# Performance work log

Measured on AMD Instinct MI355X. Metric: run time of the kernel, lower is better.

The kernel has to match this reference:

```python
import jax, jax.numpy as jnp
import numpy as np

B, T, D = 4, 4096, 256
N_SCALES, N_EXPERTS = 3, 4
KERNELS = [5, 9, 17]           # kernel bank, one group of N_EXPERTS experts per size
E = N_SCALES * N_EXPERTS       # 12 total experts
EPS = 1e-5


def _dw_causal_conv(x, w):
    """Depthwise causal conv over time. x:[B,T,D], w:[k,D] -> [B,T,D]."""
    k = w.shape[0]
    xp = jnp.pad(x, ((0, 0), (k - 1, 0), (0, 0)))
    return jax.lax.conv_general_dilated(
        xp, w[:, None, :], window_strides=(1,), padding='VALID',
        dimension_numbers=('NWC', 'WIO', 'NWC'), feature_group_count=x.shape[-1])


def setup_inputs() -> dict:
    key = jax.random.key(0)
    ks = jax.random.split(key, 12)
    s = 0.02
    return {
        'x':       jax.random.normal(ks[0], (B, T, D), jnp.float32),
        'conv_k5':  jax.random.normal(ks[1], (N_EXPERTS, 5, D), jnp.float32) * s,
        'conv_k9':  jax.random.normal(ks[2], (N_EXPERTS, 9, D), jnp.float32) * s,
        'conv_k17': jax.random.normal(ks[3], (N_EXPERTS, 17, D), jnp.float32) * s,
        'proj_W':   jax.random.normal(ks[4], (E, D, D), jnp.float32) * s,
        'proj_b':   jnp.zeros((E, D), jnp.float32),
        'router_W': jax.random.normal(ks[5], (D, E), jnp.float32) * s,
        'router_b': jnp.zeros((E,), jnp.float32),
        'out_W':    jax.random.normal(ks[6], (D, D), jnp.float32) * s,
        'out_b':    jnp.zeros((D,), jnp.float32),
        'gamma':    jnp.ones((D,), jnp.float32),
        'beta':     jnp.zeros((D,), jnp.float32),
    }


def reference(x, conv_k5, conv_k9, conv_k17, proj_W, proj_b,
              router_W, router_b, out_W, out_b, gamma, beta):
    # per-scale expert SSM (causal depthwise conv), vmapped over the 4 experts per size
    ssm_out = jnp.concatenate([
        jax.vmap(lambda w: _dw_causal_conv(x, w))(conv_k5),
        jax.vmap(lambda w: _dw_causal_conv(x, w))(conv_k9),
        jax.vmap(lambda w: _dw_causal_conv(x, w))(conv_k17),
    ], axis=0)                                             # [E,B,T,D]
    # per-expert linear projection -> [B,T,E,D]
    stack = jnp.einsum('ebtd,edf->btef', ssm_out, proj_W) + proj_b
    # router: convex combination over E experts per token
    weights = jax.nn.softmax(x @ router_W + router_b, axis=-1)   # [B,T,E]
    mixed = jnp.einsum('btef,bte->btf', stack, weights)          # [B,T,D]
    # LayerNorm
    mu = jnp.mean(mixed, axis=-1, keepdims=True)
    var = jnp.var(mixed, axis=-1, keepdims=True)
    normed = (mixed - mu) * jax.lax.rsqrt(var + EPS) * gamma + beta
    return normed @ out_W + out_b
```

## Files before the change

### kernel.cpp

```cpp
#include <hip/hip_runtime.h>
#include <hip/hip_bf16.h>

typedef short short8 __attribute__((ext_vector_type(8)));
typedef short short4_t __attribute__((ext_vector_type(4)));
typedef float floatx4 __attribute__((ext_vector_type(4)));

#define DEVI __device__ __forceinline__


DEVI float bf2f(__hip_bfloat16 v) { return __bfloat162float(v); }
DEVI __hip_bfloat16 f2bf(float v) { return __float2bfloat16(v); }
DEVI unsigned short bfbits(float v) { __hip_bfloat16 b = f2bf(v); return *(unsigned short*)&b; }

__global__ __launch_bounds__(256) void prep_kernel(
    const float* __restrict__ rW,
    const float* __restrict__ projW,
    const float* __restrict__ outW,
    const float* __restrict__ projb,
    __hip_bfloat16* __restrict__ projWT,
    __hip_bfloat16* __restrict__ outWT,
    __hip_bfloat16* __restrict__ projbT,
    __hip_bfloat16* __restrict__ rWT)
{
    __shared__ __align__(16) __hip_bfloat16 Tt[64 * 72];
    const int bid = blockIdx.x;
    const int tid = threadIdx.x;

    if (bid == 208) {
#pragma unroll
        for (int k = 0; k < 32; k++)
            projbT[tid * 32 + k] = (k < 12) ? f2bf(projb[k * 256 + tid]) : f2bf(0.f);
#pragma unroll
        for (int e = 0; e < 16; e++)
            rWT[e * 256 + tid] = (e < 12) ? f2bf(rW[tid * 12 + e]) : f2bf(0.f);
        return;
    }
    const float* src;
    __hip_bfloat16* dst;
    if (bid < 192) {
        int e = bid >> 4, ti = (bid & 15) >> 2, tj = bid & 3;
        src = projW + (e << 16) + (ti * 64) * 256 + tj * 64;
        dst = projWT + (e << 16) + (tj * 64) * 256 + ti * 64;
    } else {
        int b3 = bid - 192, ti = b3 >> 2, tj = b3 & 3;
        src = outW + (ti * 64) * 256 + tj * 64;
        dst = outWT + (tj * 64) * 256 + ti * 64;
    }
#pragma unroll
    for (int i = 0; i < 4; i++) {
        int r = i * 16 + (tid >> 4);
        int c4 = (tid & 15) * 4;
        float4 f = *(const float4*)(src + r * 256 + c4);
        Tt[(c4 + 0) * 72 + r] = f2bf(f.x);
        Tt[(c4 + 1) * 72 + r] = f2bf(f.y);
        Tt[(c4 + 2) * 72 + r] = f2bf(f.z);
        Tt[(c4 + 3) * 72 + r] = f2bf(f.w);
    }
    __syncthreads();
#pragma unroll
    for (int i = 0; i < 2; i++) {
        int c = i * 32 + (tid >> 3);
        int r8 = (tid & 7) * 8;
        *(short8*)(dst + c * 256 + r8) = *(const short8*)(Tt + c * 72 + r8);
    }
}

constexpr int SMEM_BYTES = 118016;

template<int K>
DEVI void conv_lds2(const float2 (&cf)[17], const unsigned* __restrict__ xsu,
                    int tloc, int du, const float4 (&wt4)[4],
                    unsigned* __restrict__ dp)
{
    unsigned w[16];
#pragma unroll
    for (int i = 0; i < K - 1; i++)
        w[i] = xsu[(16 + tloc - (K - 1) + i) * 132 + du];
#pragma unroll
    for (int t = 0; t < 16; t++) {
        unsigned nv = xsu[(16 + tloc + t) * 132 + du];
        float y0 = cf[K - 1].x * __uint_as_float(nv << 16);
        float y1 = cf[K - 1].y * __uint_as_float(nv & 0xffff0000u);
#pragma unroll
        for (int i = 0; i < K - 1; i++) {
            y0 = fmaf(cf[i].x, __uint_as_float(w[i] << 16), y0);
            y1 = fmaf(cf[i].y, __uint_as_float(w[i] & 0xffff0000u), y1);
        }
        float wt = wt4[t >> 2][t & 3];
        unsigned pv = ((unsigned)bfbits(y1 * wt) << 16) | (unsigned)bfbits(y0 * wt);
        dp[t * 132] = pv;
#pragma unroll
        for (int i = 0; i + 1 < K - 1; i++) w[i] = w[i + 1];
        if (K > 1) w[K - 2] = nv;
    }
}

template<int NKS>
DEVI void gemm_inl(const __hip_bfloat16* __restrict__ A, int astride,
                   const __hip_bfloat16* __restrict__ Bg, int bstride,
                   floatx4 (&acc)[4][2], int l16, int quad, int nsl)
{
    const __hip_bfloat16* ap = A + l16 * astride + quad * 8;
    const __hip_bfloat16* bp = Bg + (nsl + l16) * bstride + quad * 8;
    short8 a[4], b[2];
#pragma unroll
    for (int mf = 0; mf < 4; mf++) a[mf] = *(const short8*)(ap + mf * 16 * astride);
#pragma unroll
    for (int nt = 0; nt < 2; nt++) b[nt] = *(const short8*)(bp + nt * 16 * bstride);
#pragma unroll
    for (int ks = 0; ks < NKS; ks++) {
        short8 na[4], nb[2];
        if (ks < NKS - 1) {
#pragma unroll
            for (int mf = 0; mf < 4; mf++)
                na[mf] = *(const short8*)(ap + mf * 16 * astride + (ks + 1) * 32);
#pragma unroll
            for (int nt = 0; nt < 2; nt++)
                nb[nt] = *(const short8*)(bp + nt * 16 * bstride + (ks + 1) * 32);
        }
#pragma unroll
        for (int nt = 0; nt < 2; nt++)
#pragma unroll
            for (int mf = 0; mf < 4; mf++)
                acc[mf][nt] = __builtin_amdgcn_mfma_f32_16x16x32_bf16(
                    a[mf], b[nt], acc[mf][nt], 0, 0, 0);
        if (ks < NKS - 1) {
#pragma unroll
            for (int mf = 0; mf < 4; mf++) a[mf] = na[mf];
#pragma unroll
            for (int nt = 0; nt < 2; nt++) b[nt] = nb[nt];
        }
    }
}

__global__ __launch_bounds__(512, 1) void fused_kernel(
    const float* __restrict__ x,
    const float* __restrict__ ck5, const float* __restrict__ ck9,
    const float* __restrict__ ck17,
    const float* __restrict__ rb,
    const float* __restrict__ gmm, const float* __restrict__ bta,
    const float* __restrict__ outb,
    const __hip_bfloat16* __restrict__ projWT,
    const __hip_bfloat16* __restrict__ outWT,
    const __hip_bfloat16* __restrict__ projbT,
    const __hip_bfloat16* __restrict__ rWT,
    float* __restrict__ out)
{
    extern __shared__ char smem[];
    __hip_bfloat16* xs   = (__hip_bfloat16*)smem;
    __hip_bfloat16* bufA = (__hip_bfloat16*)(smem + 42240);
    __hip_bfloat16* bufB = (__hip_bfloat16*)(smem + 76032);
    float* wts_s = (float*)(smem + 109824);
    float* psum  = (float*)(smem + 112896);
    float* psq   = (float*)(smem + 115200);
    float* muA   = (float*)(smem + 117504);
    float* rsA   = (float*)(smem + 117760);
    const unsigned* xsu = (const unsigned*)xs;

    const int tid  = threadIdx.x;
    const int wave = tid >> 6;
    const int lane = tid & 63;
    const int quad = lane >> 4;
    const int l16  = lane & 15;
    const int nsl  = wave * 32;
    const bool gemmFirst = (wave >= 4);
    const int m0   = blockIdx.x * 64;
    const int bb   = m0 >> 12;
    const int t0   = m0 & 4095;

    {
        const float* xb = x + (size_t)bb * 4096 * 256;
        for (int idx = tid; idx < 80 * 64; idx += 512) {
            int row = idx >> 6, c4 = (idx & 63) << 2;
            int gt = t0 - 16 + row;
            short4_t v = {0, 0, 0, 0};
            if (gt >= 0) {
                float4 f = *(const float4*)(xb + (size_t)gt * 256 + c4);
                v[0] = (short)bfbits(f.x); v[1] = (short)bfbits(f.y);
                v[2] = (short)bfbits(f.z); v[3] = (short)bfbits(f.w);
            }
            *(short4_t*)(xs + row * 264 + c4) = v;
        }
    }
    __syncthreads();

    if (wave < 4) {
        floatx4 ra = {0.f, 0.f, 0.f, 0.f};
        const __hip_bfloat16* ap = xs + (16 + wave * 16 + l16) * 264 + quad * 8;
        const __hip_bfloat16* bp = rWT + l16 * 256 + quad * 8;
#pragma unroll
        for (int kk = 0; kk < 256; kk += 32)
            ra = __builtin_amdgcn_mfma_f32_16x16x32_bf16(
                *(const short8*)(ap + kk), *(const short8*)(bp + kk), ra, 0, 0, 0);
        float rbv = (l16 < 12) ? rb[l16] : 0.f;
#pragma unroll
        for (int r = 0; r < 4; r++) {
            float v = (l16 < 12) ? (ra[r] + rbv) : -1e30f;
            float mx = v;
            mx = fmaxf(mx, __shfl_xor(mx, 1));
            mx = fmaxf(mx, __shfl_xor(mx, 2));
            mx = fmaxf(mx, __shfl_xor(mx, 4));
            mx = fmaxf(mx, __shfl_xor(mx, 8));
            float ex = (l16 < 12) ? __expf(v - mx) : 0.f;
            float sm = ex;
            sm += __shfl_xor(sm, 1);
            sm += __shfl_xor(sm, 2);
            sm += __shfl_xor(sm, 4);
            sm += __shfl_xor(sm, 8);
            if (l16 < 12) wts_s[l16 * 64 + (wave * 16 + quad * 4 + r)] = ex / sm;
        }
    }
    __syncthreads();

    const int d0   = 2 * (tid & 127);
    const int du   = d0 >> 1;
    const int tloc = (tid >> 7) * 16;

    auto loadCoef = [&](float2 (&cf)[17], int e) {
        if (e < 4) {
            const float* cw = ck5 + e * 5 * 256;
#pragma unroll
            for (int j = 0; j < 17; j++)
                cf[j] = (j < 5) ? *(const float2*)(cw + j * 256 + d0) : make_float2(0.f, 0.f);
        } else if (e < 8) {
            const float* cw = ck9 + (e - 4) * 9 * 256;
#pragma unroll
            for (int j = 0; j < 17; j++)
                cf[j] = (j < 9) ? *(const float2*)(cw + j * 256 + d0) : make_float2(0.f, 0.f);
        } else {
            const float* cw = ck17 + (e - 8) * 17 * 256;
#pragma unroll
            for (int j = 0; j < 17; j++)
                cf[j] = *(const float2*)(cw + j * 256 + d0);
        }
    };
    auto produce = [&](int e, __hip_bfloat16* dst) {
        float2 cf[17];
        loadCoef(cf, e);
        float4 wt4[4];
#pragma unroll
        for (int g = 0; g < 4; g++)
            wt4[g] = *(const float4*)(wts_s + e * 64 + tloc + 4 * g);
        unsigned* dp = (unsigned*)dst + tloc * 132 + du;
        if (e < 4)      conv_lds2<5>(cf, xsu, tloc, du, wt4, dp);
        else if (e < 8) conv_lds2<9>(cf, xsu, tloc, du, wt4, dp);
        else            conv_lds2<17>(cf, xsu, tloc, du, wt4, dp);
    };
    auto produceBias = [&](__hip_bfloat16* dst) {
        int t = tid >> 3, k4 = (tid & 7) * 4;
        short4_t v;
#pragma unroll
        for (int j = 0; j < 4; j++) {
            int k = k4 + j;
            v[j] = (k < 12) ? (short)bfbits(wts_s[k * 64 + t]) : (short)0;
        }
        *(short4_t*)(dst + t * 264 + k4) = v;
    };

    floatx4 acc[4][2];
#pragma unroll
    for (int i = 0; i < 4; i++)
#pragma unroll
        for (int j = 0; j < 2; j++) acc[i][j] = {0.f, 0.f, 0.f, 0.f};

    __hip_bfloat16* bufC = bufA;
    __hip_bfloat16* bufN = bufB;

    produce(0, bufC);
    __syncthreads();

#pragma unroll 1
    for (int r = 0; r < 11; r++) {
        const __hip_bfloat16* Bg = projWT + ((size_t)r << 16);
        if (gemmFirst) {
            gemm_inl<8>(bufC, 264, Bg, 256, acc, l16, quad, nsl);
            produce(r + 1, bufN);
        } else {
            produce(r + 1, bufN);
            gemm_inl<8>(bufC, 264, Bg, 256, acc, l16, quad, nsl);
        }
        { __hip_bfloat16* t_ = bufC; bufC = bufN; bufN = t_; }
        __syncthreads();
    }
    {
        const __hip_bfloat16* Bg = projWT + ((size_t)11 << 16);
        if (gemmFirst) {
            gemm_inl<8>(bufC, 264, Bg, 256, acc, l16, quad, nsl);
            produceBias(bufN);
        } else {
            produceBias(bufN);
            gemm_inl<8>(bufC, 264, Bg, 256, acc, l16, quad, nsl);
        }
        { __hip_bfloat16* t_ = bufC; bufC = bufN; bufN = t_; }
        __syncthreads();
    }
    gemm_inl<1>(bufC, 264, projbT, 32, acc, l16, quad, nsl);

    {
        float s[16], s2[16];
#pragma unroll
        for (int mf = 0; mf < 4; mf++)
#pragma unroll
            for (int r = 0; r < 4; r++) {
                int i = mf * 4 + r;
                float v = 0.f, q = 0.f;
#pragma unroll
                for (int nt = 0; nt < 2; nt++) {
                    float a = acc[mf][nt][r];
                    v += a; q += a * a;
                }
                s[i] = v; s2[i] = q;
            }
#pragma unroll
        for (int m = 1; m <= 8; m <<= 1)
#pragma unroll
            for (int i = 0; i < 16; i++) {
                s[i]  += __shfl_xor(s[i], m);
                s2[i] += __shfl_xor(s2[i], m);
            }
#pragma unroll
        for (int i = 0; i < 16; i++)
            if (l16 == i) {
                int row = (i >> 2) * 16 + quad * 4 + (i & 3);
                psum[row * 9 + wave] = s[i];
                psq[row * 9 + wave]  = s2[i];
            }
    }
    __syncthreads();
    if (tid < 64) {
        float ss = 0.f, qq = 0.f;
#pragma unroll
        for (int p = 0; p < 8; p++) { ss += psum[tid * 9 + p]; qq += psq[tid * 9 + p]; }
        float mu = ss * 0.00390625f;
        float var = fmaxf(qq * 0.00390625f - mu * mu, 0.f);
        muA[tid] = mu;
        rsA[tid] = rsqrtf(var + 1e-5f);
    }
    __syncthreads();

    __hip_bfloat16* normed = bufN;
#pragma unroll
    for (int nt = 0; nt < 2; nt++) {
        int col = nsl + nt * 16 + l16;
        float g = gmm[col], bt = bta[col];
#pragma unroll
        for (int mf = 0; mf < 4; mf++)
#pragma unroll
            for (int r = 0; r < 4; r++) {
                int row = mf * 16 + quad * 4 + r;
                normed[row * 264 + col] =
                    f2bf((acc[mf][nt][r] - muA[row]) * rsA[row] * g + bt);
            }
    }
    __syncthreads();

    floatx4 acc2[4][2];
#pragma unroll
    for (int i = 0; i < 4; i++)
#pragma unroll
        for (int j = 0; j < 2; j++) acc2[i][j] = {0.f, 0.f, 0.f, 0.f};
    gemm_inl<8>(normed, 264, outWT, 256, acc2, l16, quad, nsl);

    float* op = out + (size_t)m0 * 256;
#pragma unroll
    for (int nt = 0; nt < 2; nt++) {
        int col = nsl + nt * 16 + l16;
        float ob = outb[col];
#pragma unroll
        for (int mf = 0; mf < 4; mf++)
#pragma unroll
            for (int r = 0; r < 4; r++) {
                int row = mf * 16 + quad * 4 + r;
                op[row * 256 + col] = acc2[mf][nt][r] + ob;
            }
    }
}

extern "C" void kernel_launch(void* const* d_in, const int* in_sizes, int n_in,
                              void* d_out, int out_size, void* d_ws, size_t ws_size,
                              hipStream_t stream)
{
    (void)in_sizes; (void)n_in; (void)out_size; (void)ws_size;
    const float* x     = (const float*)d_in[0];
    const float* ck5   = (const float*)d_in[1];
    const float* ck9   = (const float*)d_in[2];
    const float* ck17  = (const float*)d_in[3];
    const float* projW = (const float*)d_in[4];
    const float* projb = (const float*)d_in[5];
    const float* rW    = (const float*)d_in[6];
    const float* rb    = (const float*)d_in[7];
    const float* outW  = (const float*)d_in[8];
    const float* outb  = (const float*)d_in[9];
    const float* gmm   = (const float*)d_in[10];
    const float* bta   = (const float*)d_in[11];

    __hip_bfloat16* projWT = (__hip_bfloat16*)d_ws;
    __hip_bfloat16* outWT  = (__hip_bfloat16*)((char*)d_ws + 1572864);
    __hip_bfloat16* projbT = (__hip_bfloat16*)((char*)d_ws + 1703936);
    __hip_bfloat16* rWT    = (__hip_bfloat16*)((char*)d_ws + 1720320);

    static bool attr_set = false;
    if (!attr_set) {
        hipFuncSetAttribute((const void*)fused_kernel,
                            hipFuncAttributeMaxDynamicSharedMemorySize, SMEM_BYTES);
        attr_set = true;
    }

    prep_kernel<<<dim3(209), dim3(256), 0, stream>>>(
        rW, projW, outW, projb, projWT, outWT, projbT, rWT);
    fused_kernel<<<dim3(256), dim3(512), SMEM_BYTES, stream>>>(
        x, ck5, ck9, ck17, rb, gmm, bta, outb,
        projWT, outWT, projbT, rWT, (float*)d_out);
}
```

Baseline: 174.6 us.

## Double block size to 1024 threads, splitting GEMM M rows and conv time rows

Launches the fused kernel with 16 waves instead of 8. Each wave now owns a 32x32 output tile (the M dimension is split into two halves) instead of 64x32, and each conv thread processes 8 timesteps instead of 16. The aim is more latency hiding and parallelism per CU, since only 256 blocks run, one per CU. In exchange, each wave does less work per B-fragment load, so B-operand traffic from global/L2 is duplicated across the two M halves, and the register budget per thread shrinks.

After: 221.2 us. 1.27x slower.

```diff
diff --git a/kernel.cpp b/kernel.cpp
--- a/kernel.cpp
+++ b/kernel.cpp
@@ -67,9 +67,9 @@
 
 constexpr int SMEM_BYTES = 118016;
 
-template<int K>
+template<int K, int NT>
 DEVI void conv_lds2(const float2 (&cf)[17], const unsigned* __restrict__ xsu,
-                    int tloc, int du, const float4 (&wt4)[4],
+                    int tloc, int du, const float4 (&wt4)[NT / 4],
                     unsigned* __restrict__ dp)
 {
     unsigned w[16];
@@ -77,7 +77,7 @@
     for (int i = 0; i < K - 1; i++)
         w[i] = xsu[(16 + tloc - (K - 1) + i) * 132 + du];
 #pragma unroll
-    for (int t = 0; t < 16; t++) {
+    for (int t = 0; t < NT; t++) {
         unsigned nv = xsu[(16 + tloc + t) * 132 + du];
         float y0 = cf[K - 1].x * __uint_as_float(nv << 16);
         float y1 = cf[K - 1].y * __uint_as_float(nv & 0xffff0000u);
@@ -98,21 +98,21 @@
 template<int NKS>
 DEVI void gemm_inl(const __hip_bfloat16* __restrict__ A, int astride,
                    const __hip_bfloat16* __restrict__ Bg, int bstride,
-                   floatx4 (&acc)[4][2], int l16, int quad, int nsl)
+                   floatx4 (&acc)[2][2], int l16, int quad, int mh, int ns)
 {
-    const __hip_bfloat16* ap = A + l16 * astride + quad * 8;
-    const __hip_bfloat16* bp = Bg + (nsl + l16) * bstride + quad * 8;
-    short8 a[4], b[2];
-#pragma unroll
-    for (int mf = 0; mf < 4; mf++) a[mf] = *(const short8*)(ap + mf * 16 * astride);
+    const __hip_bfloat16* ap = A + (mh * 32 + l16) * astride + quad * 8;
+    const __hip_bfloat16* bp = Bg + (ns * 32 + l16) * bstride + quad * 8;
+    short8 a[2], b[2];
+#pragma unroll
+    for (int mf = 0; mf < 2; mf++) a[mf] = *(const short8*)(ap + mf * 16 * astride);
 #pragma unroll
     for (int nt = 0; nt < 2; nt++) b[nt] = *(const short8*)(bp + nt * 16 * bstride);
 #pragma unroll
     for (int ks = 0; ks < NKS; ks++) {
-        short8 na[4], nb[2];
+        short8 na[2], nb[2];
         if (ks < NKS - 1) {
 #pragma unroll
-            for (int mf = 0; mf < 4; mf++)
+            for (int mf = 0; mf < 2; mf++)
                 na[mf] = *(const short8*)(ap + mf * 16 * astride + (ks + 1) * 32);
 #pragma unroll
             for (int nt = 0; nt < 2; nt++)
@@ -121,19 +121,19 @@
 #pragma unroll
         for (int nt = 0; nt < 2; nt++)
 #pragma unroll
-            for (int mf = 0; mf < 4; mf++)
+            for (int mf = 0; mf < 2; mf++)
                 acc[mf][nt] = __builtin_amdgcn_mfma_f32_16x16x32_bf16(
                     a[mf], b[nt], acc[mf][nt], 0, 0, 0);
         if (ks < NKS - 1) {
 #pragma unroll
-            for (int mf = 0; mf < 4; mf++) a[mf] = na[mf];
+            for (int mf = 0; mf < 2; mf++) a[mf] = na[mf];
 #pragma unroll
             for (int nt = 0; nt < 2; nt++) b[nt] = nb[nt];
         }
     }
 }
 
-__global__ __launch_bounds__(512, 1) void fused_kernel(
+__global__ __launch_bounds__(1024, 1) void fused_kernel(
     const float* __restrict__ x,
     const float* __restrict__ ck5, const float* __restrict__ ck9,
     const float* __restrict__ ck17,
@@ -162,15 +162,16 @@
     const int lane = tid & 63;
     const int quad = lane >> 4;
     const int l16  = lane & 15;
-    const int nsl  = wave * 32;
-    const bool gemmFirst = (wave >= 4);
+    const int mh   = wave >> 3;
+    const int ns   = wave & 7;
+    const bool gemmFirst = ((wave >> 2) & 1);
     const int m0   = blockIdx.x * 64;
     const int bb   = m0 >> 12;
     const int t0   = m0 & 4095;
 
     {
         const float* xb = x + (size_t)bb * 4096 * 256;
-        for (int idx = tid; idx < 80 * 64; idx += 512) {
+        for (int idx = tid; idx < 80 * 64; idx += 1024) {
             int row = idx >> 6, c4 = (idx & 63) << 2;
             int gt = t0 - 16 + row;
             short4_t v = {0, 0, 0, 0};
@@ -214,7 +215,7 @@
 
     const int d0   = 2 * (tid & 127);
     const int du   = d0 >> 1;
-    const int tloc = (tid >> 7) * 16;
+    const int tloc = (tid >> 7) * 8;
 
     auto loadCoef = [&](float2 (&cf)[17], int e) {
         if (e < 4) {
@@ -237,29 +238,31 @@
     auto produce = [&](int e, __hip_bfloat16* dst) {
         float2 cf[17];
         loadCoef(cf, e);
-        float4 wt4[4];
-#pragma unroll
-        for (int g = 0; g < 4; g++)
+        float4 wt4[2];
+#pragma unroll
+        for (int g = 0; g < 2; g++)
             wt4[g] = *(const float4*)(wts_s + e * 64 + tloc + 4 * g);
         unsigned* dp = (unsigned*)dst + tloc * 132 + du;
-        if (e < 4)      conv_lds2<5>(cf, xsu, tloc, du, wt4, dp);
-        else if (e < 8) conv_lds2<9>(cf, xsu, tloc, du, wt4, dp);
-        else            conv_lds2<17>(cf, xsu, tloc, du, wt4, dp);
+        if (e < 4)      conv_lds2<5, 8>(cf, xsu, tloc, du, wt4, dp);
+        else if (e < 8) conv_lds2<9, 8>(cf, xsu, tloc, du, wt4, dp);
+        else            conv_lds2<17, 8>(cf, xsu, tloc, du, wt4, dp);
     };
     auto produceBias = [&](__hip_bfloat16* dst) {
-        int t = tid >> 3, k4 = (tid & 7) * 4;
-        short4_t v;
-#pragma unroll
-        for (int j = 0; j < 4; j++) {
-            int k = k4 + j;
-            v[j] = (k < 12) ? (short)bfbits(wts_s[k * 64 + t]) : (short)0;
-        }
-        *(short4_t*)(dst + t * 264 + k4) = v;
+        if (tid < 512) {
+            int t = tid >> 3, k4 = (tid & 7) * 4;
+            short4_t v;
+#pragma unroll
+            for (int j = 0; j < 4; j++) {
+                int k = k4 + j;
+                v[j] = (k < 12) ? (short)bfbits(wts_s[k * 64 + t]) : (short)0;
+            }
+            *(short4_t*)(dst + t * 264 + k4) = v;
+        }
     };
 
-    floatx4 acc[4][2];
-#pragma unroll
-    for (int i = 0; i < 4; i++)
+    floatx4 acc[2][2];
+#pragma unroll
+    for (int i = 0; i < 2; i++)
 #pragma unroll
         for (int j = 0; j < 2; j++) acc[i][j] = {0.f, 0.f, 0.f, 0.f};
 
@@ -273,11 +276,11 @@
     for (int r = 0; r < 11; r++) {
         const __hip_bfloat16* Bg = projWT + ((size_t)r << 16);
         if (gemmFirst) {
-            gemm_inl<8>(bufC, 264, Bg, 256, acc, l16, quad, nsl);
+            gemm_inl<8>(bufC, 264, Bg, 256, acc, l16, quad, mh, ns);
             produce(r + 1, bufN);
         } else {
             produce(r + 1, bufN);
-            gemm_inl<8>(bufC, 264, Bg, 256, acc, l16, quad, nsl);
+            gemm_inl<8>(bufC, 264, Bg, 256, acc, l16, quad, mh, ns);
         }
         { __hip_bfloat16* t_ = bufC; bufC = bufN; bufN = t_; }
         __syncthreads();
@@ -285,21 +288,21 @@
     {
         const __hip_bfloat16* Bg = projWT + ((size_t)11 << 16);
         if (gemmFirst) {
-            gemm_inl<8>(bufC, 264, Bg, 256, acc, l16, quad, nsl);
+            gemm_inl<8>(bufC, 264, Bg, 256, acc, l16, quad, mh, ns);
             produceBias(bufN);
         } else {
             produceBias(bufN);
-            gemm_inl<8>(bufC, 264, Bg, 256, acc, l16, quad, nsl);
+            gemm_inl<8>(bufC, 264, Bg, 256, acc, l16, quad, mh, ns);
         }
         { __hip_bfloat16* t_ = bufC; bufC = bufN; bufN = t_; }
         __syncthreads();
     }
-    gemm_inl<1>(bufC, 264, projbT, 32, acc, l16, quad, nsl);
+    gemm_inl<1>(bufC, 264, projbT, 32, acc, l16, quad, mh, ns);
 
     {
-        float s[16], s2[16];
-#pragma unroll
-        for (int mf = 0; mf < 4; mf++)
+        float s[8], s2[8];
+#pragma unroll
+        for (int mf = 0; mf < 2; mf++)
 #pragma unroll
             for (int r = 0; r < 4; r++) {
                 int i = mf * 4 + r;
@@ -314,16 +317,16 @@
 #pragma unroll
         for (int m = 1; m <= 8; m <<= 1)
 #pragma unroll
-            for (int i = 0; i < 16; i++) {
+            for (int i = 0; i < 8; i++) {
                 s[i]  += __shfl_xor(s[i], m);
                 s2[i] += __shfl_xor(s2[i], m);
             }
 #pragma unroll
-        for (int i = 0; i < 16; i++)
+        for (int i = 0; i < 8; i++)
             if (l16 == i) {
-                int row = (i >> 2) * 16 + quad * 4 + (i & 3);
-                psum[row * 9 + wave] = s[i];
-                psq[row * 9 + wave]  = s2[i];
+                int row = mh * 32 + (i >> 2) * 16 + quad * 4 + (i & 3);
+                psum[row * 9 + ns] = s[i];
+                psq[row * 9 + ns]  = s2[i];
             }
     }
     __syncthreads();
@@ -341,36 +344,36 @@
     __hip_bfloat16* normed = bufN;
 #pragma unroll
     for (int nt = 0; nt < 2; nt++) {
-        int col = nsl + nt * 16 + l16;
+        int col = ns * 32 + nt * 16 + l16;
         float g = gmm[col], bt = bta[col];
 #pragma unroll
-        for (int mf = 0; mf < 4; mf++)
+        for (int mf = 0; mf < 2; mf++)
 #pragma unroll
             for (int r = 0; r < 4; r++) {
-                int row = mf * 16 + quad * 4 + r;
+                int row = mh * 32 + mf * 16 + quad * 4 + r;
                 normed[row * 264 + col] =
                     f2bf((acc[mf][nt][r] - muA[row]) * rsA[row] * g + bt);
             }
     }
     __syncthreads();
 
-    floatx4 acc2[4][2];
-#pragma unroll
-    for (int i = 0; i < 4; i++)
+    floatx4 acc2[2][2];
+#pragma unroll
+    for (int i = 0; i < 2; i++)
 #pragma unroll
         for (int j = 0; j < 2; j++) acc2[i][j] = {0.f, 0.f, 0.f, 0.f};
-    gemm_inl<8>(normed, 264, outWT, 256, acc2, l16, quad, nsl);
+    gemm_inl<8>(normed, 264, outWT, 256, acc2, l16, quad, mh, ns);
 
     float* op = out + (size_t)m0 * 256;
 #pragma unroll
     for (int nt = 0; nt < 2; nt++) {
-        int col = nsl + nt * 16 + l16;
+        int col = ns * 32 + nt * 16 + l16;
         float ob = outb[col];
 #pragma unroll
-        for (int mf = 0; mf < 4; mf++)
+        for (int mf = 0; mf < 2; mf++)
 #pragma unroll
             for (int r = 0; r < 4; r++) {
-                int row = mf * 16 + quad * 4 + r;
+                int row = mh * 32 + mf * 16 + quad * 4 + r;
                 op[row * 256 + col] = acc2[mf][nt][r] + ob;
             }
     }
@@ -408,7 +411,7 @@
 
     prep_kernel<<<dim3(209), dim3(256), 0, stream>>>(
         rW, projW, outW, projb, projWT, outWT, projbT, rWT);
-    fused_kernel<<<dim3(256), dim3(512), SMEM_BYTES, stream>>>(
+    fused_kernel<<<dim3(256), dim3(1024), SMEM_BYTES, stream>>>(
         x, ck5, ck9, ck17, rb, gmm, bta, outb,
         projWT, outWT, projbT, rWT, (float*)d_out);
 }
```

## Halve row tile to 32 with 256-thread blocks and drop double buffering

Applied to the files above, without the earlier changes.

Shrinks each block from 64 rows/512 threads to 32 rows/256 threads, doubling the grid to 512 blocks. The per-wave tile changes from 4x2 to 2x4 MFMA fragments. The double-buffered produce/GEMM overlap across wave groups is replaced by a single LDS buffer with two barriers per expert, so LDS drops to about 45KB and two blocks can share a CU. This trades intra-block overlap of conv and GEMM for more resident blocks and better CU coverage. It also doubles how often the projection weights are re-read per token.

Result: slower. 208.0 us (+19.1%).

```diff
diff --git a/kernel.cpp b/kernel.cpp
--- a/kernel.cpp
+++ b/kernel.cpp
@@ -65,7 +65,6 @@
     }
 }
 
-constexpr int SMEM_BYTES = 118016;
 
 template<int K>
 DEVI void conv_lds2(const float2 (&cf)[17], const unsigned* __restrict__ xsu,
@@ -98,42 +97,42 @@
 template<int NKS>
 DEVI void gemm_inl(const __hip_bfloat16* __restrict__ A, int astride,
                    const __hip_bfloat16* __restrict__ Bg, int bstride,
-                   floatx4 (&acc)[4][2], int l16, int quad, int nsl)
+                   floatx4 (&acc)[2][4], int l16, int quad, int nsl)
 {
     const __hip_bfloat16* ap = A + l16 * astride + quad * 8;
     const __hip_bfloat16* bp = Bg + (nsl + l16) * bstride + quad * 8;
-    short8 a[4], b[2];
-#pragma unroll
-    for (int mf = 0; mf < 4; mf++) a[mf] = *(const short8*)(ap + mf * 16 * astride);
-#pragma unroll
-    for (int nt = 0; nt < 2; nt++) b[nt] = *(const short8*)(bp + nt * 16 * bstride);
+    short8 a[2], b[4];
+#pragma unroll
+    for (int mf = 0; mf < 2; mf++) a[mf] = *(const short8*)(ap + mf * 16 * astride);
+#pragma unroll
+    for (int nt = 0; nt < 4; nt++) b[nt] = *(const short8*)(bp + nt * 16 * bstride);
 #pragma unroll
     for (int ks = 0; ks < NKS; ks++) {
-        short8 na[4], nb[2];
+        short8 na[2], nb[4];
         if (ks < NKS - 1) {
 #pragma unroll
-            for (int mf = 0; mf < 4; mf++)
+            for (int mf = 0; mf < 2; mf++)
                 na[mf] = *(const short8*)(ap + mf * 16 * astride + (ks + 1) * 32);
 #pragma unroll
-            for (int nt = 0; nt < 2; nt++)
+            for (int nt = 0; nt < 4; nt++)
                 nb[nt] = *(const short8*)(bp + nt * 16 * bstride + (ks + 1) * 32);
         }
 #pragma unroll
-        for (int nt = 0; nt < 2; nt++)
-#pragma unroll
-            for (int mf = 0; mf < 4; mf++)
+        for (int nt = 0; nt < 4; nt++)
+#pragma unroll
+            for (int mf = 0; mf < 2; mf++)
                 acc[mf][nt] = __builtin_amdgcn_mfma_f32_16x16x32_bf16(
                     a[mf], b[nt], acc[mf][nt], 0, 0, 0);
         if (ks < NKS - 1) {
 #pragma unroll
-            for (int mf = 0; mf < 4; mf++) a[mf] = na[mf];
-#pragma unroll
-            for (int nt = 0; nt < 2; nt++) b[nt] = nb[nt];
-        }
-    }
-}
-
-__global__ __launch_bounds__(512, 1) void fused_kernel(
+            for (int mf = 0; mf < 2; mf++) a[mf] = na[mf];
+#pragma unroll
+            for (int nt = 0; nt < 4; nt++) b[nt] = nb[nt];
+        }
+    }
+}
+
+__global__ __launch_bounds__(256, 2) void fused_kernel(
     const float* __restrict__ x,
     const float* __restrict__ ck5, const float* __restrict__ ck9,
     const float* __restrict__ ck17,
@@ -146,15 +145,15 @@
     const __hip_bfloat16* __restrict__ rWT,
     float* __restrict__ out)
 {
-    extern __shared__ char smem[];
-    __hip_bfloat16* xs   = (__hip_bfloat16*)smem;
-    __hip_bfloat16* bufA = (__hip_bfloat16*)(smem + 42240);
-    __hip_bfloat16* bufB = (__hip_bfloat16*)(smem + 76032);
-    float* wts_s = (float*)(smem + 109824);
-    float* psum  = (float*)(smem + 112896);
-    float* psq   = (float*)(smem + 115200);
-    float* muA   = (float*)(smem + 117504);
-    float* rsA   = (float*)(smem + 117760);
+    __shared__ __align__(16) char smem[45312];
+    __hip_bfloat16* xs = (__hip_bfloat16*)smem;
+    __hip_bfloat16* As = (__hip_bfloat16*)(smem + 25344);
+    float* wts_s = (float*)(smem + 42240);
+    float* psum  = (float*)(smem + 43776);
+    float* psq   = (float*)(smem + 44416);
+    float* muA   = (float*)(smem + 45056);
+    float* rsA   = (float*)(smem + 45184);
+    __hip_bfloat16* normed = (__hip_bfloat16*)smem;
     const unsigned* xsu = (const unsigned*)xs;
 
     const int tid  = threadIdx.x;
@@ -162,15 +161,14 @@
     const int lane = tid & 63;
     const int quad = lane >> 4;
     const int l16  = lane & 15;
-    const int nsl  = wave * 32;
-    const bool gemmFirst = (wave >= 4);
-    const int m0   = blockIdx.x * 64;
+    const int nsl  = wave * 64;
+    const int m0   = blockIdx.x * 32;
     const int bb   = m0 >> 12;
     const int t0   = m0 & 4095;
 
     {
         const float* xb = x + (size_t)bb * 4096 * 256;
-        for (int idx = tid; idx < 80 * 64; idx += 512) {
+        for (int idx = tid; idx < 48 * 64; idx += 256) {
             int row = idx >> 6, c4 = (idx & 63) << 2;
             int gt = t0 - 16 + row;
             short4_t v = {0, 0, 0, 0};
@@ -184,7 +182,7 @@
     }
     __syncthreads();
 
-    if (wave < 4) {
+    if (wave < 2) {
         floatx4 ra = {0.f, 0.f, 0.f, 0.f};
         const __hip_bfloat16* ap = xs + (16 + wave * 16 + l16) * 264 + quad * 8;
         const __hip_bfloat16* bp = rWT + l16 * 256 + quad * 8;
@@ -207,7 +205,7 @@
             sm += __shfl_xor(sm, 2);
             sm += __shfl_xor(sm, 4);
             sm += __shfl_xor(sm, 8);
-            if (l16 < 12) wts_s[l16 * 64 + (wave * 16 + quad * 4 + r)] = ex / sm;
+            if (l16 < 12) wts_s[l16 * 32 + (wave * 16 + quad * 4 + r)] = ex / sm;
         }
     }
     __syncthreads();
@@ -234,78 +232,58 @@
                 cf[j] = *(const float2*)(cw + j * 256 + d0);
         }
     };
-    auto produce = [&](int e, __hip_bfloat16* dst) {
+    auto produce = [&](int e) {
         float2 cf[17];
         loadCoef(cf, e);
         float4 wt4[4];
 #pragma unroll
         for (int g = 0; g < 4; g++)
-            wt4[g] = *(const float4*)(wts_s + e * 64 + tloc + 4 * g);
-        unsigned* dp = (unsigned*)dst + tloc * 132 + du;
+            wt4[g] = *(const float4*)(wts_s + e * 32 + tloc + 4 * g);
+        unsigned* dp = (unsigned*)As + tloc * 132 + du;
         if (e < 4)      conv_lds2<5>(cf, xsu, tloc, du, wt4, dp);
         else if (e < 8) conv_lds2<9>(cf, xsu, tloc, du, wt4, dp);
         else            conv_lds2<17>(cf, xsu, tloc, du, wt4, dp);
     };
-    auto produceBias = [&](__hip_bfloat16* dst) {
+    auto produceBias = [&]() {
         int t = tid >> 3, k4 = (tid & 7) * 4;
         short4_t v;
 #pragma unroll
         for (int j = 0; j < 4; j++) {
             int k = k4 + j;
-            v[j] = (k < 12) ? (short)bfbits(wts_s[k * 64 + t]) : (short)0;
-        }
-        *(short4_t*)(dst + t * 264 + k4) = v;
+            v[j] = (k < 12) ? (short)bfbits(wts_s[k * 32 + t]) : (short)0;
+        }
+        *(short4_t*)(As + t * 264 + k4) = v;
     };
 
-    floatx4 acc[4][2];
-#pragma unroll
-    for (int i = 0; i < 4; i++)
-#pragma unroll
-        for (int j = 0; j < 2; j++) acc[i][j] = {0.f, 0.f, 0.f, 0.f};
-
-    __hip_bfloat16* bufC = bufA;
-    __hip_bfloat16* bufN = bufB;
-
-    produce(0, bufC);
+    floatx4 acc[2][4];
+#pragma unroll
+    for (int i = 0; i < 2; i++)
+#pragma unroll
+        for (int j = 0; j < 4; j++) acc[i][j] = {0.f, 0.f, 0.f, 0.f};
+
+    produce(0);
     __syncthreads();
 
 #pragma unroll 1
-    for (int r = 0; r < 11; r++) {
-        const __hip_bfloat16* Bg = projWT + ((size_t)r << 16);
-        if (gemmFirst) {
-            gemm_inl<8>(bufC, 264, Bg, 256, acc, l16, quad, nsl);
-            produce(r + 1, bufN);
-        } else {
-            produce(r + 1, bufN);
-            gemm_inl<8>(bufC, 264, Bg, 256, acc, l16, quad, nsl);
-        }
-        { __hip_bfloat16* t_ = bufC; bufC = bufN; bufN = t_; }
+    for (int e = 0; e < 12; e++) {
+        gemm_inl<8>(As, 264, projWT + ((size_t)e << 16), 256, acc, l16, quad, nsl);
         __syncthreads();
-    }
+        if (e < 11) produce(e + 1);
+        else        produceBias();
+        __syncthreads();
+    }
+    gemm_inl<1>(As, 264, projbT, 32, acc, l16, quad, nsl);
+
     {
-        const __hip_bfloat16* Bg = projWT + ((size_t)11 << 16);
-        if (gemmFirst) {
-            gemm_inl<8>(bufC, 264, Bg, 256, acc, l16, quad, nsl);
-            produceBias(bufN);
-        } else {
-            produceBias(bufN);
-            gemm_inl<8>(bufC, 264, Bg, 256, acc, l16, quad, nsl);
-        }
-        { __hip_bfloat16* t_ = bufC; bufC = bufN; bufN = t_; }
-        __syncthreads();
-    }
-    gemm_inl<1>(bufC, 264, projbT, 32, acc, l16, quad, nsl);
-
-    {
-        float s[16], s2[16];
-#pragma unroll
-        for (int mf = 0; mf < 4; mf++)
+        float s[8], s2[8];
+#pragma unroll
+        for (int mf = 0; mf < 2; mf++)
 #pragma unroll
             for (int r = 0; r < 4; r++) {
                 int i = mf * 4 + r;
                 float v = 0.f, q = 0.f;
 #pragma unroll
-                for (int nt = 0; nt < 2; nt++) {
+                for (int nt = 0; nt < 4; nt++) {
                     float a = acc[mf][nt][r];
                     v += a; q += a * a;
                 }
@@ -314,23 +292,23 @@
 #pragma unroll
         for (int m = 1; m <= 8; m <<= 1)
 #pragma unroll
-            for (int i = 0; i < 16; i++) {
+            for (int i = 0; i < 8; i++) {
                 s[i]  += __shfl_xor(s[i], m);
                 s2[i] += __shfl_xor(s2[i], m);
             }
 #pragma unroll
-        for (int i = 0; i < 16; i++)
+        for (int i = 0; i < 8; i++)
             if (l16 == i) {
                 int row = (i >> 2) * 16 + quad * 4 + (i & 3);
-                psum[row * 9 + wave] = s[i];
-                psq[row * 9 + wave]  = s2[i];
-            }
-    }
-    __syncthreads();
-    if (tid < 64) {
+                psum[row * 5 + wave] = s[i];
+                psq[row * 5 + wave]  = s2[i];
+            }
+    }
+    __syncthreads();
+    if (tid < 32) {
         float ss = 0.f, qq = 0.f;
 #pragma unroll
-        for (int p = 0; p < 8; p++) { ss += psum[tid * 9 + p]; qq += psq[tid * 9 + p]; }
+        for (int p = 0; p < 4; p++) { ss += psum[tid * 5 + p]; qq += psq[tid * 5 + p]; }
         float mu = ss * 0.00390625f;
         float var = fmaxf(qq * 0.00390625f - mu * mu, 0.f);
         muA[tid] = mu;
@@ -338,13 +316,12 @@
     }
     __syncthreads();
 
-    __hip_bfloat16* normed = bufN;
-#pragma unroll
-    for (int nt = 0; nt < 2; nt++) {
+#pragma unroll
+    for (int nt = 0; nt < 4; nt++) {
         int col = nsl + nt * 16 + l16;
         float g = gmm[col], bt = bta[col];
 #pragma unroll
-        for (int mf = 0; mf < 4; mf++)
+        for (int mf = 0; mf < 2; mf++)
 #pragma unroll
             for (int r = 0; r < 4; r++) {
                 int row = mf * 16 + quad * 4 + r;
@@ -354,20 +331,20 @@
     }
     __syncthreads();
 
-    floatx4 acc2[4][2];
-#pragma unroll
-    for (int i = 0; i < 4; i++)
-#pragma unroll
-        for (int j = 0; j < 2; j++) acc2[i][j] = {0.f, 0.f, 0.f, 0.f};
+    floatx4 acc2[2][4];
+#pragma unroll
+    for (int i = 0; i < 2; i++)
+#pragma unroll
+        for (int j = 0; j < 4; j++) acc2[i][j] = {0.f, 0.f, 0.f, 0.f};
     gemm_inl<8>(normed, 264, outWT, 256, acc2, l16, quad, nsl);
 
     float* op = out + (size_t)m0 * 256;
 #pragma unroll
-    for (int nt = 0; nt < 2; nt++) {
+    for (int nt = 0; nt < 4; nt++) {
         int col = nsl + nt * 16 + l16;
         float ob = outb[col];
 #pragma unroll
-        for (int mf = 0; mf < 4; mf++)
+        for (int mf = 0; mf < 2; mf++)
 #pragma unroll
             for (int r = 0; r < 4; r++) {
                 int row = mf * 16 + quad * 4 + r;
@@ -399,16 +376,9 @@
     __hip_bfloat16* projbT = (__hip_bfloat16*)((char*)d_ws + 1703936);
     __hip_bfloat16* rWT    = (__hip_bfloat16*)((char*)d_ws + 1720320);
 
-    static bool attr_set = false;
-    if (!attr_set) {
-        hipFuncSetAttribute((const void*)fused_kernel,
-                            hipFuncAttributeMaxDynamicSharedMemorySize, SMEM_BYTES);
-        attr_set = true;
-    }
-
     prep_kernel<<<dim3(209), dim3(256), 0, stream>>>(
         rW, projW, outW, projb, projWT, outWT, projbT, rWT);
-    fused_kernel<<<dim3(256), dim3(512), SMEM_BYTES, stream>>>(
+    fused_kernel<<<dim3(512), dim3(256), 0, stream>>>(
         x, ck5, ck9, ck17, rb, gmm, bta, outb,
         projWT, outWT, projbT, rWT, (float*)d_out);
 }
```
